# Kernel tuning notes

Hardware: AMD Instinct MI355X
Metric: run time of the kernel (lower is better)

The kernel has to match this reference:

```python
import jax, jax.numpy as jnp
import numpy as np

HEADS = 8
DIM_HEAD = 64


def setup_inputs() -> dict:
    key = jax.random.key(0)
    ks = jax.random.split(key, 10)
    B, NQ, NK, D, INNER = 4, 2048, 2048, 1024, HEADS * DIM_HEAD
    w_scale = 0.02
    return {
        "x": jax.random.normal(ks[0], (B, NQ, D), jnp.float32),
        "context": jax.random.normal(ks[1], (B, NK, D), jnp.float32),
        "wq": jax.random.normal(ks[2], (D, INNER), jnp.float32) * w_scale,
        "bq": jax.random.normal(ks[3], (INNER,), jnp.float32) * w_scale,
        "wk": jax.random.normal(ks[4], (D, INNER), jnp.float32) * w_scale,
        "bk": jax.random.normal(ks[5], (INNER,), jnp.float32) * w_scale,
        "wv": jax.random.normal(ks[6], (D, INNER), jnp.float32) * w_scale,
        "bv": jax.random.normal(ks[7], (INNER,), jnp.float32) * w_scale,
        "wo": jax.random.normal(ks[8], (INNER, D), jnp.float32) * w_scale,
        "bo": jax.random.normal(ks[9], (D,), jnp.float32) * w_scale,
    }


def _split_heads(t):
    # [b, n, h*d] -> [b, h, n, d]
    b, n, _ = t.shape
    return t.reshape(b, n, HEADS, DIM_HEAD).transpose(0, 2, 1, 3)


def reference(x, context, wq, bq, wk, bk, wv, bv, wo, bo):
    scale = DIM_HEAD ** -0.5
    q = _split_heads(x @ wq + bq)        # [b, h, nq, d]
    k = _split_heads(context @ wk + bk)  # [b, h, nk, d]
    v = _split_heads(context @ wv + bv)  # [b, h, nk, d]
    sim = jnp.einsum('bhid,bhjd->bhij', q, k) * scale  # full score matrix, as in original
    attn = jax.nn.softmax(sim, axis=-1)
    out = jnp.einsum('bhij,bhjd->bhid', attn, v)       # [b, h, nq, d]
    b, h, n, d = out.shape
    out = out.transpose(0, 2, 1, 3).reshape(b, n, h * d)
    return out @ wo + bo
```

## Files before the change

### kernel.cpp

```cpp
#include <hip/hip_runtime.h>
#include <hip/hip_bf16.h>

typedef __attribute__((ext_vector_type(8))) short short8;
typedef __attribute__((ext_vector_type(4))) float f32x4;
typedef __attribute__((ext_vector_type(2))) unsigned uint2u;

__device__ __forceinline__ short f2bf(float f) {
  union { float f; unsigned u; } x; x.f = f;
  unsigned r = x.u + 0x7fffu + ((x.u >> 16) & 1u);
  return (short)(r >> 16);
}

__device__ __forceinline__ unsigned cvt_pk_bf16(float a, float b) {
  unsigned r;
  asm("v_cvt_pk_bf16_f32 %0, %1, %2" : "=v"(r) : "v"(a), "v"(b));
  return r;
}

__device__ __forceinline__ float fast_exp2(float x) {
#if __has_builtin(__builtin_amdgcn_exp2f)
  return __builtin_amdgcn_exp2f(x);
#else
  return exp2f(x);
#endif
}

__device__ __forceinline__ void gload16(const short* g, short* l) {
  __builtin_amdgcn_global_load_lds(
      (const __attribute__((address_space(1))) unsigned*)g,
      (__attribute__((address_space(3))) unsigned*)l, 16, 0, 0);
}

__device__ __forceinline__ void barrier_lgkm() {
  asm volatile("s_waitcnt lgkmcnt(0)" ::: "memory");
  __builtin_amdgcn_s_barrier();
}

__global__ void cast2_bf16_kernel(const float* __restrict__ a,
                                  const float* __restrict__ b,
                                  short* __restrict__ dst) {
  int i = (blockIdx.x * 256 + threadIdx.x) * 4;
  const float* s = (i < (1 << 23)) ? a : b;
  int j = i & ((1 << 23) - 1);
  float4 f = *(const float4*)(s + j);
  union { short s[4]; uint2 u; } o;
  o.s[0] = f2bf(f.x); o.s[1] = f2bf(f.y);
  o.s[2] = f2bf(f.z); o.s[3] = f2bf(f.w);
  *(uint2*)(dst + i) = o.u;
}

__global__ __launch_bounds__(256) void transpose_cast4_kernel(
    const float* __restrict__ wq, const float* __restrict__ wk,
    const float* __restrict__ wv, const float* __restrict__ wo,
    short* __restrict__ wqt, short* __restrict__ wkt,
    short* __restrict__ wvt, short* __restrict__ wot) {
  __shared__ short tile[64][72];
  int z = blockIdx.z;
  const float* src = (z == 0) ? wq : (z == 1) ? wk : (z == 2) ? wv : wo;
  short* dst = (z == 0) ? wqt : (z == 1) ? wkt : (z == 2) ? wvt : wot;
  int R = (z < 3) ? 1024 : 512, C = (z < 3) ? 512 : 1024;
  int tpc = C >> 6;
  int bx = blockIdx.x % tpc, by = blockIdx.x / tpc;
  int r0 = by * 64, c0 = bx * 64;
  int tx = threadIdx.x & 15, ty = threadIdx.x >> 4;
#pragma unroll
  for (int i = 0; i < 4; i++) {
    int r = i * 16 + ty;
    float4 f = *(const float4*)(src + (size_t)(r0 + r) * C + c0 + tx * 4);
    union { short s[4]; uint2 u; } o;
    o.s[0] = f2bf(f.x); o.s[1] = f2bf(f.y);
    o.s[2] = f2bf(f.z); o.s[3] = f2bf(f.w);
    *(uint2*)&tile[r][tx * 4] = o.u;
  }
  __syncthreads();
#pragma unroll
  for (int i = 0; i < 4; i++) {
    int c = i * 16 + ty;
    union { short s[4]; uint2 u; } o;
#pragma unroll
    for (int k = 0; k < 4; k++) o.s[k] = tile[tx * 4 + k][c];
    *(uint2*)(dst + (size_t)(c0 + c) * R + r0 + tx * 4) = o.u;
  }
}

template <bool SWAP>
__device__ __forceinline__ void gemm_core(
    const short* __restrict__ A, const short* __restrict__ Bt, int K,
    int mblk, int nblk, short* sA, short* sB, f32x4 (&acc)[4][4]) {
  int tid = threadIdx.x;
  int lane = tid & 63, wave = tid >> 6;
  int quad = lane >> 4, l15 = lane & 15;
  int wm = (wave >> 1) * 64, wn = (wave & 1) * 64;
  int sub = lane >> 3, e8 = lane & 7;
  int swz = (e8 ^ sub) << 3;
  int s0 = (quad ^ (l15 & 7)) << 3;
  const short* Ag = A + (size_t)(mblk + 32 * wave + sub) * K + swz;
  const short* Bg = Bt + (size_t)(nblk + 32 * wave + sub) * K + swz;
  short* Al = sA + 4 * wave * 512;
  short* Bl = sB + 4 * wave * 512;

  auto STAGE = [&](int b, int k0) {
    short* a = Al + b * 8192;
    short* bb = Bl + b * 8192;
#pragma unroll
    for (int t = 0; t < 4; t++) {
      gload16(Ag + (size_t)(8 * t) * K + k0, a + t * 512);
      gload16(Bg + (size_t)(8 * t) * K + k0, bb + t * 512);
    }
  };

  int nsteps = K >> 6;
  STAGE(0, 0);
  __syncthreads();
  int buf = 0;
  for (int step = 0; step < nsteps; ++step) {
    if (step + 1 < nsteps) STAGE(buf ^ 1, (step + 1) << 6);
    const short* sAb = sA + buf * 8192;
    const short* sBb = sB + buf * 8192;
#pragma unroll
    for (int h = 0; h < 2; h++) {
      int so = s0 ^ (h << 5);
      short8 af[4], bf[4];
#pragma unroll
      for (int mt = 0; mt < 4; mt++)
        af[mt] = *(const short8*)(&sAb[(wm + mt * 16 + l15) * 64 + so]);
#pragma unroll
      for (int nt = 0; nt < 4; nt++)
        bf[nt] = *(const short8*)(&sBb[(wn + nt * 16 + l15) * 64 + so]);
#pragma unroll
      for (int mt = 0; mt < 4; mt++)
#pragma unroll
        for (int nt = 0; nt < 4; nt++) {
          if (SWAP)
            acc[mt][nt] = __builtin_amdgcn_mfma_f32_16x16x32_bf16(
                bf[nt], af[mt], acc[mt][nt], 0, 0, 0);
          else
            acc[mt][nt] = __builtin_amdgcn_mfma_f32_16x16x32_bf16(
                af[mt], bf[nt], acc[mt][nt], 0, 0, 0);
        }
    }
    __syncthreads();
    buf ^= 1;
  }
}

__global__ __launch_bounds__(256) void gemm_qkv(
    const short* __restrict__ xb, const short* __restrict__ cb,
    const short* __restrict__ wqt, const short* __restrict__ wkt,
    const short* __restrict__ wvt,
    const float* __restrict__ bq, const float* __restrict__ bk,
    const float* __restrict__ bv,
    short* __restrict__ Qb, short* __restrict__ Kb, short* __restrict__ Vt) {
  __shared__ __align__(16) short sA[2 * 128 * 64];
  __shared__ __align__(16) short sB[2 * 128 * 64];
  int z = blockIdx.z;
  const short* A  = (z == 0) ? xb : cb;
  const short* Bt = (z == 0) ? wqt : (z == 1) ? wkt : wvt;
  const float* bias = (z == 0) ? bq : (z == 1) ? bk : bv;
  short* out = (z == 0) ? Qb : (z == 1) ? Kb : Vt;
  float scale = (z == 0) ? 0.18033688011112042f : 1.0f;
  int mblk = blockIdx.x * 128, nblk = blockIdx.y * 128;
  int lane = threadIdx.x & 63, wave = threadIdx.x >> 6;
  int quad = lane >> 4, l15 = lane & 15;
  int wm = (wave >> 1) * 64, wn = (wave & 1) * 64;

  if (z == 2) {
    f32x4 acc[4][4] = {};
    gemm_core<false>(A, Bt, 1024, mblk, nblk, sA, sB, acc);
#pragma unroll
    for (int nt = 0; nt < 4; nt++) {
      int col = nblk + wn + nt * 16 + l15;
      float bias_v = bias[col];
      int h = col >> 6, dh = col & 63;
#pragma unroll
      for (int mt = 0; mt < 4; mt++) {
        int row0 = mblk + wm + mt * 16 + quad * 4;
        int b = row0 >> 11, n0 = row0 & 2047;
        size_t base = ((size_t)(b * 8 + h)) << 17;
        union { short s[4]; uint2 u; } pk;
#pragma unroll
        for (int r = 0; r < 4; r++) pk.s[r] = f2bf(acc[mt][nt][r] + bias_v);
        *(uint2*)(out + base + ((size_t)dh << 11) + n0) = pk.u;
      }
    }
  } else {
    f32x4 acc[4][4] = {};
    gemm_core<true>(A, Bt, 1024, mblk, nblk, sA, sB, acc);
#pragma unroll
    for (int nt = 0; nt < 4; nt++) {
      int colbase = nblk + wn + nt * 16 + quad * 4;
      float4 b4 = *(const float4*)(bias + colbase);
      int h = colbase >> 6, dh0 = colbase & 63;
#pragma unroll
      for (int mt = 0; mt < 4; mt++) {
        int row = mblk + wm + mt * 16 + l15;
        int b = row >> 11, n = row & 2047;
        size_t base = ((size_t)(b * 8 + h)) << 17;
        union { short s[4]; uint2 u; } pk;
        pk.s[0] = f2bf((acc[mt][nt][0] + b4.x) * scale);
        pk.s[1] = f2bf((acc[mt][nt][1] + b4.y) * scale);
        pk.s[2] = f2bf((acc[mt][nt][2] + b4.z) * scale);
        pk.s[3] = f2bf((acc[mt][nt][3] + b4.w) * scale);
        *(uint2*)(out + base + ((size_t)n << 6) + dh0) = pk.u;
      }
    }
  }
}

__global__ __launch_bounds__(256) void gemm_out(
    const short* __restrict__ Ob, const short* __restrict__ wot,
    const float* __restrict__ bo, float* __restrict__ out) {
  __shared__ __align__(16) short sA[2 * 128 * 64];
  __shared__ __align__(16) short sB[2 * 128 * 64];
  int mblk = blockIdx.x * 128, nblk = blockIdx.y * 128;
  f32x4 acc[4][4] = {};
  gemm_core<true>(Ob, wot, 512, mblk, nblk, sA, sB, acc);
  int lane = threadIdx.x & 63, wave = threadIdx.x >> 6;
  int quad = lane >> 4, l15 = lane & 15;
  int wm = (wave >> 1) * 64, wn = (wave & 1) * 64;
#pragma unroll
  for (int nt = 0; nt < 4; nt++) {
    int colbase = nblk + wn + nt * 16 + quad * 4;
    float4 b4 = *(const float4*)(bo + colbase);
#pragma unroll
    for (int mt = 0; mt < 4; mt++) {
      int row = mblk + wm + mt * 16 + l15;
      f32x4 v;
      v[0] = acc[mt][nt][0] + b4.x; v[1] = acc[mt][nt][1] + b4.y;
      v[2] = acc[mt][nt][2] + b4.z; v[3] = acc[mt][nt][3] + b4.w;
      *(f32x4*)(out + (size_t)row * 1024 + colbase) = v;
    }
  }
}

__global__ __launch_bounds__(256, 2) void attn_kernel(
    const short* __restrict__ Qb, const short* __restrict__ Kb,
    const short* __restrict__ Vt, short* __restrict__ Ob) {
  __shared__ __align__(16) short sK[2 * 64 * 64];
  __shared__ __align__(16) short sV[2 * 64 * 64];
  int tid = threadIdx.x;
  int lane = tid & 63, wave = tid >> 6;
  int quad = lane >> 4, l15 = lane & 15;
  int bh = blockIdx.x & 31;
  int qt = blockIdx.x >> 5;
  const short* Qp = Qb + ((size_t)bh << 17);
  const short* Kp = Kb + ((size_t)bh << 17);
  const short* Vp = Vt + ((size_t)bh << 17);
  int qrow0 = qt * 128 + wave * 32;

  short8 qf[2][2];
#pragma unroll
  for (int g = 0; g < 2; g++) {
    const short* qrow = Qp + (size_t)(qrow0 + g * 16 + l15) * 64;
    qf[g][0] = *(const short8*)(qrow + quad * 8);
    qf[g][1] = *(const short8*)(qrow + 32 + quad * 8);
  }

  int jk0 = 2 * wave, jk1 = 2 * wave + 1;
  int sub = lane >> 3;
  int e8  = lane & 7;
  int swz = (e8 ^ sub) << 3;
  const short* kg0 = Kp + (size_t)(8 * jk0 + sub) * 64 + e8 * 8;
  const short* kg1 = Kp + (size_t)(8 * jk1 + sub) * 64 + e8 * 8;
  const short* vg0 = Vp + (size_t)(8 * jk0 + sub) * 2048 + e8 * 8;
  const short* vg1 = Vp + (size_t)(8 * jk1 + sub) * 2048 + e8 * 8;
  int kw0 = (8 * jk0 + sub) * 64 + swz;
  int kw1 = (8 * jk1 + sub) * 64 + swz;

  int s0 = (quad ^ (l15 & 7)) << 3;
  int s1 = s0 ^ 32;

  f32x4 o[2][4] = {};
  float lsum[2] = {0.f, 0.f};

  uint4 rk0 = *(const uint4*)kg0, rk1 = *(const uint4*)kg1;
  uint4 rv0 = *(const uint4*)vg0, rv1 = *(const uint4*)vg1;
  *(uint4*)(sK + kw0) = rk0; *(uint4*)(sK + kw1) = rk1;
  *(uint4*)(sV + kw0) = rv0; *(uint4*)(sV + kw1) = rv1;
  rk0 = *(const uint4*)(kg0 + 4096); rk1 = *(const uint4*)(kg1 + 4096);
  rv0 = *(const uint4*)(vg0 + 64);   rv1 = *(const uint4*)(vg1 + 64);
  barrier_lgkm();

  for (int it = 0; it < 32; ++it) {
    const short* sKr = sK + (it & 1) * 4096;
    const short* sVr = sV + (it & 1) * 4096;
    if (it < 31) {
      short* sKw = sK + ((it & 1) ^ 1) * 4096;
      short* sVw = sV + ((it & 1) ^ 1) * 4096;
      *(uint4*)(sKw + kw0) = rk0; *(uint4*)(sKw + kw1) = rk1;
      *(uint4*)(sVw + kw0) = rv0; *(uint4*)(sVw + kw1) = rv1;
      if (it < 30) {
        size_t ko = (size_t)(it + 2) * 4096;
        size_t vo = (size_t)(it + 2) * 64;
        rk0 = *(const uint4*)(kg0 + ko); rk1 = *(const uint4*)(kg1 + ko);
        rv0 = *(const uint4*)(vg0 + vo); rv1 = *(const uint4*)(vg1 + vo);
      }
    }
    unsigned xp[2][4][2];
#pragma unroll
    for (int jt = 0; jt < 4; jt++) {
      short8 k0 = *(const short8*)(&sKr[(jt * 16 + l15) * 64 + s0]);
      short8 k1 = *(const short8*)(&sKr[(jt * 16 + l15) * 64 + s1]);
#pragma unroll
      for (int g = 0; g < 2; g++) {
        f32x4 zz = {0.f, 0.f, 0.f, 0.f};
        __builtin_amdgcn_s_setprio(1);
        zz = __builtin_amdgcn_mfma_f32_16x16x32_bf16(k0, qf[g][0], zz, 0, 0, 0);
        f32x4 st = __builtin_amdgcn_mfma_f32_16x16x32_bf16(k1, qf[g][1], zz, 0, 0, 0);
        __builtin_amdgcn_s_setprio(0);
        float p0 = fast_exp2(st[0]), p1 = fast_exp2(st[1]);
        float p2 = fast_exp2(st[2]), p3 = fast_exp2(st[3]);
        lsum[g] += (p0 + p1) + (p2 + p3);
        xp[g][jt][0] = cvt_pk_bf16(p0, p1);
        xp[g][jt][1] = cvt_pk_bf16(p2, p3);
      }
    }
    short8 pf[2][2];
#pragma unroll
    for (int g = 0; g < 2; g++) {
#pragma unroll
      for (int hb = 0; hb < 2; hb++) {
        unsigned x0 = xp[g][2 * hb][0], x1 = xp[g][2 * hb][1];
        unsigned x2 = xp[g][2 * hb + 1][0], x3 = xp[g][2 * hb + 1][1];
        uint2u r1 = __builtin_amdgcn_permlane32_swap(x0, x2, false, false);
        uint2u r2 = __builtin_amdgcn_permlane16_swap(r1[0], r1[1], false, false);
        uint2u r3 = __builtin_amdgcn_permlane32_swap(x1, x3, false, false);
        uint2u r4 = __builtin_amdgcn_permlane16_swap(r3[0], r3[1], false, false);
        union { unsigned u[4]; short8 s; } P;
        P.u[0] = r2[0]; P.u[1] = r4[0]; P.u[2] = r2[1]; P.u[3] = r4[1];
        pf[g][hb] = P.s;
      }
    }
    __builtin_amdgcn_s_setprio(1);
#pragma unroll
    for (int nt = 0; nt < 4; nt++) {
      short8 v0 = *(const short8*)(&sVr[(nt * 16 + l15) * 64 + s0]);
      short8 v1 = *(const short8*)(&sVr[(nt * 16 + l15) * 64 + s1]);
#pragma unroll
      for (int g = 0; g < 2; g++) {
        o[g][nt] = __builtin_amdgcn_mfma_f32_16x16x32_bf16(v0, pf[g][0], o[g][nt], 0, 0, 0);
        o[g][nt] = __builtin_amdgcn_mfma_f32_16x16x32_bf16(v1, pf[g][1], o[g][nt], 0, 0, 0);
      }
    }
    __builtin_amdgcn_s_setprio(0);
    if (it < 31) barrier_lgkm();
  }

  int b = bh >> 3, h = bh & 7;
#pragma unroll
  for (int g = 0; g < 2; g++) {
    float l = lsum[g];
    l += __shfl_xor(l, 16, 64);
    l += __shfl_xor(l, 32, 64);
    float inv = 1.0f / l;
    size_t rowbase = ((size_t)b * 2048 + qrow0 + g * 16 + l15) * 512 + h * 64 + quad * 4;
#pragma unroll
    for (int nt = 0; nt < 4; nt++) {
      union { short s[4]; uint2 u; } pk2;
#pragma unroll
      for (int r = 0; r < 4; r++) pk2.s[r] = f2bf(o[g][nt][r] * inv);
      *(uint2*)(Ob + rowbase + nt * 16) = pk2.u;
    }
  }
}

extern "C" void kernel_launch(void* const* d_in, const int* in_sizes, int n_in,
                              void* d_out, int out_size, void* d_ws, size_t ws_size,
                              hipStream_t stream) {
  const float* x   = (const float*)d_in[0];
  const float* ctx = (const float*)d_in[1];
  const float* wq  = (const float*)d_in[2];
  const float* bq  = (const float*)d_in[3];
  const float* wk  = (const float*)d_in[4];
  const float* bk  = (const float*)d_in[5];
  const float* wv  = (const float*)d_in[6];
  const float* bv  = (const float*)d_in[7];
  const float* wo  = (const float*)d_in[8];
  const float* bo  = (const float*)d_in[9];
  float* out = (float*)d_out;
  char* ws = (char*)d_ws;

  short* xb  = (short*)(ws);
  short* cb  = (short*)(ws + (16ull << 20));
  short* wqt = (short*)(ws + (32ull << 20));
  short* wkt = (short*)(ws + (33ull << 20));
  short* wvt = (short*)(ws + (34ull << 20));
  short* wot = (short*)(ws + (35ull << 20));
  short* Qb  = (short*)(ws + (36ull << 20));
  short* Kb  = (short*)(ws + (44ull << 20));
  short* Vt  = (short*)(ws + (52ull << 20));
  short* Ob  = (short*)(ws + (60ull << 20));

  cast2_bf16_kernel<<<16384, 256, 0, stream>>>(x, ctx, xb);
  transpose_cast4_kernel<<<dim3(128, 1, 4), 256, 0, stream>>>(
      wq, wk, wv, wo, wqt, wkt, wvt, wot);
  gemm_qkv<<<dim3(64, 4, 3), 256, 0, stream>>>(xb, cb, wqt, wkt, wvt,
                                               bq, bk, bv, Qb, Kb, Vt);
  attn_kernel<<<512, 256, 0, stream>>>(Qb, Kb, Vt, Ob);
  gemm_out<<<dim3(64, 8), 256, 0, stream>>>(Ob, wot, bo, out);
}
```

Measured before the change: 229.0 us.

## Halve attention rows per wave for higher occupancy; single-buffer output GEMM

The attention kernel now processes 16 query rows per wave (64 per block), launches twice as many blocks and requests 4 blocks per CU, to reduce register pressure and raise occupancy. The output projection GEMM uses a new single-buffered LDS loop with explicit barriers instead of double buffering, halving its shared memory. In exchange, each attention block reloads all K/V for fewer queries, doubling K/V traffic, and the GEMM loses load/compute overlap.

```diff
diff --git a/kernel.cpp b/kernel.cpp
--- a/kernel.cpp
+++ b/kernel.cpp
@@ -83,8 +83,9 @@
   }
 }
 
+
 template <bool SWAP>
-__device__ __forceinline__ void gemm_core(
+__device__ __forceinline__ void gemm_core_2ph(
     const short* __restrict__ A, const short* __restrict__ Bt, int K,
     int mblk, int nblk, short* sA, short* sB, f32x4 (&acc)[4][4]) {
   int tid = threadIdx.x;
@@ -141,6 +142,55 @@
     }
     __syncthreads();
     buf ^= 1;
+  }
+}
+
+template <bool SWAP>
+__device__ __forceinline__ void gemm_core_1buf(
+    const short* __restrict__ A, const short* __restrict__ Bt, int K,
+    int mblk, int nblk, short* sA, short* sB, f32x4 (&acc)[4][4]) {
+  int tid = threadIdx.x;
+  int lane = tid & 63, wave = tid >> 6;
+  int quad = lane >> 4, l15 = lane & 15;
+  int wm = (wave >> 1) * 64, wn = (wave & 1) * 64;
+  int sub = lane >> 3, e8 = lane & 7;
+  int swz = (e8 ^ sub) << 3;
+  int s0 = (quad ^ (l15 & 7)) << 3;
+  const short* Ag = A + (size_t)(mblk + 32 * wave + sub) * K + swz;
+  const short* Bg = Bt + (size_t)(nblk + 32 * wave + sub) * K + swz;
+  short* Al = sA + 4 * wave * 512;
+  short* Bl = sB + 4 * wave * 512;
+
+  for (int k0 = 0; k0 < K; k0 += 64) {
+    __syncthreads();
+#pragma unroll
+    for (int t = 0; t < 4; t++) {
+      gload16(Ag + (size_t)(8 * t) * K + k0, Al + t * 512);
+      gload16(Bg + (size_t)(8 * t) * K + k0, Bl + t * 512);
+    }
+    __syncthreads();
+#pragma unroll
+    for (int h = 0; h < 2; h++) {
+      int so = s0 ^ (h << 5);
+      short8 af[4], bf[4];
+#pragma unroll
+      for (int mt = 0; mt < 4; mt++)
+        af[mt] = *(const short8*)(&sA[(wm + mt * 16 + l15) * 64 + so]);
+#pragma unroll
+      for (int nt = 0; nt < 4; nt++)
+        bf[nt] = *(const short8*)(&sB[(wn + nt * 16 + l15) * 64 + so]);
+#pragma unroll
+      for (int mt = 0; mt < 4; mt++)
+#pragma unroll
+        for (int nt = 0; nt < 4; nt++) {
+          if (SWAP)
+            acc[mt][nt] = __builtin_amdgcn_mfma_f32_16x16x32_bf16(
+                bf[nt], af[mt], acc[mt][nt], 0, 0, 0);
+          else
+            acc[mt][nt] = __builtin_amdgcn_mfma_f32_16x16x32_bf16(
+                af[mt], bf[nt], acc[mt][nt], 0, 0, 0);
+        }
+    }
   }
 }
 
@@ -166,7 +216,7 @@
 
   if (z == 2) {
     f32x4 acc[4][4] = {};
-    gemm_core<false>(A, Bt, 1024, mblk, nblk, sA, sB, acc);
+    gemm_core_2ph<false>(A, Bt, 1024, mblk, nblk, sA, sB, acc);
 #pragma unroll
     for (int nt = 0; nt < 4; nt++) {
       int col = nblk + wn + nt * 16 + l15;
@@ -185,7 +235,7 @@
     }
   } else {
     f32x4 acc[4][4] = {};
-    gemm_core<true>(A, Bt, 1024, mblk, nblk, sA, sB, acc);
+    gemm_core_2ph<true>(A, Bt, 1024, mblk, nblk, sA, sB, acc);
 #pragma unroll
     for (int nt = 0; nt < 4; nt++) {
       int colbase = nblk + wn + nt * 16 + quad * 4;
@@ -210,11 +260,11 @@
 __global__ __launch_bounds__(256) void gemm_out(
     const short* __restrict__ Ob, const short* __restrict__ wot,
     const float* __restrict__ bo, float* __restrict__ out) {
-  __shared__ __align__(16) short sA[2 * 128 * 64];
-  __shared__ __align__(16) short sB[2 * 128 * 64];
+  __shared__ __align__(16) short sA[128 * 64];
+  __shared__ __align__(16) short sB[128 * 64];
   int mblk = blockIdx.x * 128, nblk = blockIdx.y * 128;
   f32x4 acc[4][4] = {};
-  gemm_core<true>(Ob, wot, 512, mblk, nblk, sA, sB, acc);
+  gemm_core_1buf<true>(Ob, wot, 512, mblk, nblk, sA, sB, acc);
   int lane = threadIdx.x & 63, wave = threadIdx.x >> 6;
   int quad = lane >> 4, l15 = lane & 15;
   int wm = (wave >> 1) * 64, wn = (wave & 1) * 64;
@@ -233,7 +283,7 @@
   }
 }
 
-__global__ __launch_bounds__(256, 2) void attn_kernel(
+__global__ __launch_bounds__(256, 4) void attn_kernel(
     const short* __restrict__ Qb, const short* __restrict__ Kb,
     const short* __restrict__ Vt, short* __restrict__ Ob) {
   __shared__ __align__(16) short sK[2 * 64 * 64];
@@ -246,15 +296,11 @@
   const short* Qp = Qb + ((size_t)bh << 17);
   const short* Kp = Kb + ((size_t)bh << 17);
   const short* Vp = Vt + ((size_t)bh << 17);
-  int qrow0 = qt * 128 + wave * 32;
-
-  short8 qf[2][2];
-#pragma unroll
-  for (int g = 0; g < 2; g++) {
-    const short* qrow = Qp + (size_t)(qrow0 + g * 16 + l15) * 64;
-    qf[g][0] = *(const short8*)(qrow + quad * 8);
-    qf[g][1] = *(const short8*)(qrow + 32 + quad * 8);
-  }
+  int qrow0 = qt * 64 + wave * 16;
+
+  const short* qrow = Qp + (size_t)(qrow0 + l15) * 64;
+  short8 qf0 = *(const short8*)(qrow + quad * 8);
+  short8 qf1 = *(const short8*)(qrow + 32 + quad * 8);
 
   int jk0 = 2 * wave, jk1 = 2 * wave + 1;
   int sub = lane >> 3;
@@ -270,8 +316,8 @@
   int s0 = (quad ^ (l15 & 7)) << 3;
   int s1 = s0 ^ 32;
 
-  f32x4 o[2][4] = {};
-  float lsum[2] = {0.f, 0.f};
+  f32x4 o[4] = {};
+  float lsum = 0.f;
 
   uint4 rk0 = *(const uint4*)kg0, rk1 = *(const uint4*)kg1;
   uint4 rv0 = *(const uint4*)vg0, rv1 = *(const uint4*)vg1;
@@ -296,71 +342,59 @@
         rv0 = *(const uint4*)(vg0 + vo); rv1 = *(const uint4*)(vg1 + vo);
       }
     }
-    unsigned xp[2][4][2];
+    unsigned xp[4][2];
 #pragma unroll
     for (int jt = 0; jt < 4; jt++) {
       short8 k0 = *(const short8*)(&sKr[(jt * 16 + l15) * 64 + s0]);
       short8 k1 = *(const short8*)(&sKr[(jt * 16 + l15) * 64 + s1]);
-#pragma unroll
-      for (int g = 0; g < 2; g++) {
-        f32x4 zz = {0.f, 0.f, 0.f, 0.f};
-        __builtin_amdgcn_s_setprio(1);
-        zz = __builtin_amdgcn_mfma_f32_16x16x32_bf16(k0, qf[g][0], zz, 0, 0, 0);
-        f32x4 st = __builtin_amdgcn_mfma_f32_16x16x32_bf16(k1, qf[g][1], zz, 0, 0, 0);
-        __builtin_amdgcn_s_setprio(0);
-        float p0 = fast_exp2(st[0]), p1 = fast_exp2(st[1]);
-        float p2 = fast_exp2(st[2]), p3 = fast_exp2(st[3]);
-        lsum[g] += (p0 + p1) + (p2 + p3);
-        xp[g][jt][0] = cvt_pk_bf16(p0, p1);
-        xp[g][jt][1] = cvt_pk_bf16(p2, p3);
-      }
-    }
-    short8 pf[2][2];
-#pragma unroll
-    for (int g = 0; g < 2; g++) {
-#pragma unroll
-      for (int hb = 0; hb < 2; hb++) {
-        unsigned x0 = xp[g][2 * hb][0], x1 = xp[g][2 * hb][1];
-        unsigned x2 = xp[g][2 * hb + 1][0], x3 = xp[g][2 * hb + 1][1];
-        uint2u r1 = __builtin_amdgcn_permlane32_swap(x0, x2, false, false);
-        uint2u r2 = __builtin_amdgcn_permlane16_swap(r1[0], r1[1], false, false);
-        uint2u r3 = __builtin_amdgcn_permlane32_swap(x1, x3, false, false);
-        uint2u r4 = __builtin_amdgcn_permlane16_swap(r3[0], r3[1], false, false);
-        union { unsigned u[4]; short8 s; } P;
-        P.u[0] = r2[0]; P.u[1] = r4[0]; P.u[2] = r2[1]; P.u[3] = r4[1];
-        pf[g][hb] = P.s;
-      }
+      f32x4 zz = {0.f, 0.f, 0.f, 0.f};
+      __builtin_amdgcn_s_setprio(1);
+      zz = __builtin_amdgcn_mfma_f32_16x16x32_bf16(k0, qf0, zz, 0, 0, 0);
+      f32x4 st = __builtin_amdgcn_mfma_f32_16x16x32_bf16(k1, qf1, zz, 0, 0, 0);
+      __builtin_amdgcn_s_setprio(0);
+      float p0 = fast_exp2(st[0]), p1 = fast_exp2(st[1]);
+      float p2 = fast_exp2(st[2]), p3 = fast_exp2(st[3]);
+      lsum += (p0 + p1) + (p2 + p3);
+      xp[jt][0] = cvt_pk_bf16(p0, p1);
+      xp[jt][1] = cvt_pk_bf16(p2, p3);
+    }
+    short8 pf[2];
+#pragma unroll
+    for (int hb = 0; hb < 2; hb++) {
+      unsigned x0 = xp[2 * hb][0], x1 = xp[2 * hb][1];
+      unsigned x2 = xp[2 * hb + 1][0], x3 = xp[2 * hb + 1][1];
+      uint2u r1 = __builtin_amdgcn_permlane32_swap(x0, x2, false, false);
+      uint2u r2 = __builtin_amdgcn_permlane16_swap(r1[0], r1[1], false, false);
+      uint2u r3 = __builtin_amdgcn_permlane32_swap(x1, x3, false, false);
+      uint2u r4 = __builtin_amdgcn_permlane16_swap(r3[0], r3[1], false, false);
+      union { unsigned u[4]; short8 s; } P;
+      P.u[0] = r2[0]; P.u[1] = r4[0]; P.u[2] = r2[1]; P.u[3] = r4[1];
+      pf[hb] = P.s;
     }
     __builtin_amdgcn_s_setprio(1);
 #pragma unroll
     for (int nt = 0; nt < 4; nt++) {
       short8 v0 = *(const short8*)(&sVr[(nt * 16 + l15) * 64 + s0]);
       short8 v1 = *(const short8*)(&sVr[(nt * 16 + l15) * 64 + s1]);
-#pragma unroll
-      for (int g = 0; g < 2; g++) {
-        o[g][nt] = __builtin_amdgcn_mfma_f32_16x16x32_bf16(v0, pf[g][0], o[g][nt], 0, 0, 0);
-        o[g][nt] = __builtin_amdgcn_mfma_f32_16x16x32_bf16(v1, pf[g][1], o[g][nt], 0, 0, 0);
-      }
+      o[nt] = __builtin_amdgcn_mfma_f32_16x16x32_bf16(v0, pf[0], o[nt], 0, 0, 0);
+      o[nt] = __builtin_amdgcn_mfma_f32_16x16x32_bf16(v1, pf[1], o[nt], 0, 0, 0);
     }
     __builtin_amdgcn_s_setprio(0);
     if (it < 31) barrier_lgkm();
   }
 
   int b = bh >> 3, h = bh & 7;
-#pragma unroll
-  for (int g = 0; g < 2; g++) {
-    float l = lsum[g];
-    l += __shfl_xor(l, 16, 64);
-    l += __shfl_xor(l, 32, 64);
-    float inv = 1.0f / l;
-    size_t rowbase = ((size_t)b * 2048 + qrow0 + g * 16 + l15) * 512 + h * 64 + quad * 4;
-#pragma unroll
-    for (int nt = 0; nt < 4; nt++) {
-      union { short s[4]; uint2 u; } pk2;
-#pragma unroll
-      for (int r = 0; r < 4; r++) pk2.s[r] = f2bf(o[g][nt][r] * inv);
-      *(uint2*)(Ob + rowbase + nt * 16) = pk2.u;
-    }
+  float l = lsum;
+  l += __shfl_xor(l, 16, 64);
+  l += __shfl_xor(l, 32, 64);
+  float inv = 1.0f / l;
+  size_t rowbase = ((size_t)b * 2048 + qrow0 + l15) * 512 + h * 64 + quad * 4;
+#pragma unroll
+  for (int nt = 0; nt < 4; nt++) {
+    union { short s[4]; uint2 u; } pk2;
+#pragma unroll
+    for (int r = 0; r < 4; r++) pk2.s[r] = f2bf(o[nt][r] * inv);
+    *(uint2*)(Ob + rowbase + nt * 16) = pk2.u;
   }
 }
 
@@ -396,6 +430,6 @@
       wq, wk, wv, wo, wqt, wkt, wvt, wot);
   gemm_qkv<<<dim3(64, 4, 3), 256, 0, stream>>>(xb, cb, wqt, wkt, wvt,
                                                bq, bk, bv, Qb, Kb, Vt);
-  attn_kernel<<<512, 256, 0, stream>>>(Qb, Kb, Vt, Ob);
+  attn_kernel<<<1024, 256, 0, stream>>>(Qb, Kb, Vt, Ob);
   gemm_out<<<dim3(64, 8), 256, 0, stream>>>(Ob, wot, bo, out);
 }
```

Result: no change. 231.5 us (+1.1%).
